# Performance work log

Measured on AMD Instinct MI355X. Metric: run time of the kernel, lower is better.

Reference implementation:

```python
import jax, jax.numpy as jnp
import numpy as np

D_MODEL = 1024
NHEAD = 16
HEAD_DIM = D_MODEL // NHEAD
D_FF = 4096
EPS = 1e-5


def _layer_norm(x, gamma, beta):
    mu = jnp.mean(x, axis=-1, keepdims=True)
    var = jnp.mean((x - mu) ** 2, axis=-1, keepdims=True)
    return (x - mu) * jax.lax.rsqrt(var + EPS) * gamma + beta


def setup_inputs() -> dict:
    key = jax.random.key(0)
    ks = jax.random.split(key, 12)
    B, S = 2, 2048
    s = lambda fan_in: 1.0 / np.sqrt(fan_in)
    return {
        "src": jax.random.normal(ks[0], (B, S, D_MODEL), dtype=jnp.float32),
        "attn_bias": jax.random.normal(ks[1], (NHEAD, S, S), dtype=jnp.float32) * 0.02,
        "qkv_w": jax.random.uniform(ks[2], (3 * D_MODEL, D_MODEL), minval=-s(D_MODEL), maxval=s(D_MODEL)),
        "qkv_b": jax.random.uniform(ks[3], (3 * D_MODEL,), minval=-s(D_MODEL), maxval=s(D_MODEL)),
        "out_w": jax.random.uniform(ks[4], (D_MODEL, D_MODEL), minval=-s(D_MODEL), maxval=s(D_MODEL)),
        "out_b": jax.random.uniform(ks[5], (D_MODEL,), minval=-s(D_MODEL), maxval=s(D_MODEL)),
        "lin1_w": jax.random.uniform(ks[6], (D_FF, D_MODEL), minval=-s(D_MODEL), maxval=s(D_MODEL)),
        "lin1_b": jax.random.uniform(ks[7], (D_FF,), minval=-s(D_MODEL), maxval=s(D_MODEL)),
        "lin2_w": jax.random.uniform(ks[8], (D_MODEL, D_FF), minval=-s(D_FF), maxval=s(D_FF)),
        "lin2_b": jax.random.uniform(ks[9], (D_MODEL,), minval=-s(D_FF), maxval=s(D_FF)),
        "ln1_g": jnp.ones((D_MODEL,)), "ln1_b": jnp.zeros((D_MODEL,)),
        "ln2_g": jnp.ones((D_MODEL,)), "ln2_b": jnp.zeros((D_MODEL,)),
    }


def reference(src, attn_bias, qkv_w, qkv_b, out_w, out_b, lin1_w, lin1_b,
              lin2_w, lin2_b, ln1_g, ln1_b, ln2_g, ln2_b):
    B, S, _ = src.shape
    qkv = src @ qkv_w.T + qkv_b                      # [B,S,3D]
    q, k, v = jnp.split(qkv, 3, axis=-1)
    q = q.reshape(B, S, NHEAD, HEAD_DIM)
    k = k.reshape(B, S, NHEAD, HEAD_DIM)
    v = v.reshape(B, S, NHEAD, HEAD_DIM)
    scores = jnp.einsum('bthd,bshd->bhts', q, k) / np.sqrt(HEAD_DIM)
    scores = scores + attn_bias[None]                # 3D bias -> broadcast over batch
    weights = jax.nn.softmax(scores, axis=-1)
    ctx = jnp.einsum('bhts,bshd->bthd', weights, v).reshape(B, S, D_MODEL)
    attn_out = ctx @ out_w.T + out_b
    x = _layer_norm(src + attn_out, ln1_g, ln1_b)
    ff = jax.nn.gelu(x @ lin1_w.T + lin1_b, approximate=False) @ lin2_w.T + lin2_b
    return _layer_norm(x + ff, ln2_g, ln2_b)
```

## Files before the change

kernel.cpp:

```cpp
#include <hip/hip_runtime.h>
#include <hip/hip_bf16.h>


#define DMODEL 1024
#define NHEAD  16
#define HD     64
#define DFF    4096
#define SEQ    2048
#define BATCH  2
#define TOKD   ((size_t)4096 * 1024)

using short8 = __attribute__((ext_vector_type(8))) short;
using f32x4  = __attribute__((ext_vector_type(4))) float;
typedef unsigned short bfu;

__device__ __forceinline__ bfu f2bf(float f) {
    unsigned int u = __float_as_uint(f);
    unsigned int r = (u + 0x7fffu + ((u >> 16) & 1u)) >> 16;
    return (bfu)r;
}

__device__ __forceinline__ float gelu_exact(float x) {
    return 0.5f * x * (1.0f + erff(x * 0.70710678118654752f));
}

__device__ __forceinline__ void gload16(const void* g, void* l) {
    __builtin_amdgcn_global_load_lds(
        (const __attribute__((address_space(1))) void*)g,
        (__attribute__((address_space(3))) void*)l, 16, 0, 0);
}

__device__ __forceinline__ int swz(int row, int colbyte) {
    return (row * 128 + colbyte) ^ ((row & 7) << 4);
}

__global__ __launch_bounds__(256) void cvt_f32_bf16(const float* __restrict__ in,
                                                    bfu* __restrict__ out, int n4) {
    int i = blockIdx.x * 256 + threadIdx.x;
    if (i >= n4) return;
    float4 v = *(const float4*)(in + (size_t)i * 4);
    uint2 o;
    o.x = (unsigned)f2bf(v.x) | ((unsigned)f2bf(v.y) << 16);
    o.y = (unsigned)f2bf(v.z) | ((unsigned)f2bf(v.w) << 16);
    *(uint2*)(out + (size_t)i * 4) = o;
}

template <int MODE, int BM, int SPLITK>
__global__ __launch_bounds__(256) void gemm_bt(const bfu* __restrict__ A,
                                               const bfu* __restrict__ W,
                                               const float* __restrict__ bias,
                                               void* __restrict__ Cout,
                                               int M, int N, int K) {
    constexpr int MR = BM / 32;
    __shared__ __align__(16) bfu As[BM * 32];
    __shared__ __align__(16) bfu Bs[128 * 32];
    const int tid = threadIdx.x;
    const int wid = tid >> 6, lane = tid & 63;
    const int lg = lane >> 4, li = lane & 15;

    const int nx = gridDim.x;
    int wg = blockIdx.x + nx * blockIdx.y;
    const int nwg = nx * gridDim.y;
    {
        const int qq = nwg >> 3, rr = nwg & 7;
        const int xcd = wg & 7, idx = wg >> 3;
        wg = (xcd < rr ? xcd * (qq + 1) : rr * (qq + 1) + (xcd - rr) * qq) + idx;
    }
    const int row0 = (wg % nx) * BM, col0 = (wg / nx) * 128;
    const int wr = (wid >> 1) * (BM / 2), wc = (wid & 1) * 64;
    f32x4 acc[MR][4] = {};

    const int kchunk = K / SPLITK;
    const int kbeg = blockIdx.z * kchunk;

    const int ch_row = tid >> 2;
    const int ch_col = (tid & 3) * 8;
    const bfu* Ag0 = A + (size_t)(row0 + ch_row) * K + kbeg + ch_col;
    const bfu* Ag1 = A + (size_t)(row0 + 64 + ch_row) * K + kbeg + ch_col;
    const bfu* Wg0 = W + (size_t)(col0 + ch_row) * K + kbeg + ch_col;
    const bfu* Wg1 = W + (size_t)(col0 + 64 + ch_row) * K + kbeg + ch_col;
    char* Al0 = (char*)As + wid * 1024;
    char* Al1 = (char*)As + 4096 + wid * 1024;
    char* Bl0 = (char*)Bs + wid * 1024;
    char* Bl1 = (char*)Bs + 4096 + wid * 1024;

    for (int k0 = 0; k0 < kchunk; k0 += 32) {
        gload16(Ag0 + k0, Al0);
        if constexpr (BM == 128) gload16(Ag1 + k0, Al1);
        gload16(Wg0 + k0, Bl0);
        gload16(Wg1 + k0, Bl1);
        __syncthreads();
        short8 af[MR], bf_[4];
        #pragma unroll
        for (int m = 0; m < MR; ++m)
            af[m] = *(const short8*)(As + (wr + m * 16 + li) * 32 + lg * 8);
        #pragma unroll
        for (int n = 0; n < 4; ++n)
            bf_[n] = *(const short8*)(Bs + (wc + n * 16 + li) * 32 + lg * 8);
        #pragma unroll
        for (int m = 0; m < MR; ++m)
            #pragma unroll
            for (int n = 0; n < 4; ++n)
                acc[m][n] = __builtin_amdgcn_mfma_f32_16x16x32_bf16(af[m], bf_[n], acc[m][n], 0, 0, 0);
        __syncthreads();
    }

    float* Cp3 = (float*)Cout + (size_t)blockIdx.z * M * N;
    #pragma unroll
    for (int m = 0; m < MR; ++m) {
        #pragma unroll
        for (int n = 0; n < 4; ++n) {
            #pragma unroll
            for (int r = 0; r < 4; ++r) {
                int row = row0 + wr + m * 16 + lg * 4 + r;
                int col = col0 + wc + n * 16 + li;
                if (MODE == 3) {
                    Cp3[(size_t)row * N + col] = acc[m][n][r];
                } else {
                    float v = acc[m][n][r] + bias[col];
                    if (MODE == 2) v = gelu_exact(v);
                    ((bfu*)Cout)[(size_t)row * N + col] = f2bf(v);
                }
            }
        }
    }
}

__global__ __launch_bounds__(256) void attn_kernel(const bfu* __restrict__ qkv,
                                                   const float* __restrict__ bias,
                                                   bfu* __restrict__ ctx) {
    __shared__ __align__(16) bfu Ks[128 * 64];
    __shared__ __align__(16) bfu Vt[2][64 * 64];
    __shared__ __align__(16) bfu Ps[4][16 * 64];
    const int tid = threadIdx.x;
    const int wid = tid >> 6, lane = tid & 63;
    const int lg = lane >> 4, li = lane & 15;
    const int q0 = blockIdx.x * 64;
    const int bh = blockIdx.y;
    const int h = bh >> 1, b = bh & 1;
    const size_t tokbase = (size_t)b * SEQ;

    short8 qa[2];
    {
        const bfu* qp = qkv + (tokbase + q0 + wid * 16 + li) * 3072 + h * 64;
        qa[0] = *(const short8*)(qp + lg * 8);
        qa[1] = *(const short8*)(qp + 32 + lg * 8);
    }

    f32x4 o[4] = {};
    float mrow[4], lrow[4];
    #pragma unroll
    for (int r = 0; r < 4; ++r) { mrow[r] = -1e30f; lrow[r] = 0.f; }

    char* pb = (char*)Ps[wid];
    const float* brow = bias + (size_t)h * SEQ * SEQ;
    const int qrbase = q0 + wid * 16 + lg * 4;

    const int krow  = tid >> 3;
    const int kcolb = (tid & 7) * 16;

    for (int kt = 0; kt < SEQ; kt += 128) {
        #pragma unroll
        for (int p = 0; p < 4; ++p) {
            int r_ = p * 32 + krow;
            uint4 v = *(const uint4*)(qkv + (tokbase + kt + r_) * 3072 + 1024 + h * 64 + (kcolb >> 1));
            *(uint4*)((char*)Ks + swz(r_, kcolb)) = v;
        }
        #pragma unroll
        for (int jh = 0; jh < 2; ++jh) {
            #pragma unroll
            for (int i = 0; i < 2; ++i) {
                int jb = i * 4 + wid;
                bfu tmp[8];
                #pragma unroll
                for (int u = 0; u < 8; ++u)
                    tmp[u] = qkv[(tokbase + kt + jh * 64 + jb * 8 + u) * 3072 + 2048 + h * 64 + lane];
                uint4 pv;
                pv.x = (unsigned)tmp[0] | ((unsigned)tmp[1] << 16);
                pv.y = (unsigned)tmp[2] | ((unsigned)tmp[3] << 16);
                pv.z = (unsigned)tmp[4] | ((unsigned)tmp[5] << 16);
                pv.w = (unsigned)tmp[6] | ((unsigned)tmp[7] << 16);
                *(uint4*)((char*)Vt[jh] + swz(lane, jb * 16)) = pv;
            }
        }
        __syncthreads();

        float breg[4][8];
        #pragma unroll
        for (int r = 0; r < 4; ++r) {
            const float* bq = brow + (size_t)(qrbase + r) * SEQ + kt;
            #pragma unroll
            for (int nb = 0; nb < 8; ++nb)
                breg[r][nb] = bq[nb * 16 + li];
        }

        f32x4 s[8] = {};
        __builtin_amdgcn_s_setprio(1);
        #pragma unroll
        for (int cb = 0; cb < 2; ++cb) {
            #pragma unroll
            for (int nb = 0; nb < 8; ++nb) {
                short8 kf = *(const short8*)((char*)Ks + swz(nb * 16 + li, cb * 64 + lg * 16));
                s[nb] = __builtin_amdgcn_mfma_f32_16x16x32_bf16(qa[cb], kf, s[nb], 0, 0, 0);
            }
        }
        __builtin_amdgcn_s_setprio(0);

        #pragma unroll
        for (int r = 0; r < 4; ++r) {
            float sv[8];
            float mx = -1e30f;
            #pragma unroll
            for (int nb = 0; nb < 8; ++nb) {
                float v = s[nb][r] * 0.125f + breg[r][nb];
                sv[nb] = v;
                mx = fmaxf(mx, v);
            }
            #pragma unroll
            for (int off = 8; off; off >>= 1) mx = fmaxf(mx, __shfl_xor(mx, off));
            float mnew = fmaxf(mrow[r], mx);
            float sf = __expf(mrow[r] - mnew);
            mrow[r] = mnew;
            float rs = 0.f;
            #pragma unroll
            for (int nb = 0; nb < 8; ++nb) {
                float p = __expf(sv[nb] - mnew);
                rs += p;
                s[nb][r] = p;
            }
            #pragma unroll
            for (int off = 8; off; off >>= 1) rs += __shfl_xor(rs, off);
            lrow[r] = lrow[r] * sf + rs;
            #pragma unroll
            for (int dc = 0; dc < 4; ++dc) o[dc][r] *= sf;
        }

        #pragma unroll
        for (int jh = 0; jh < 2; ++jh) {
            #pragma unroll
            for (int nb = 0; nb < 4; ++nb)
                #pragma unroll
                for (int r = 0; r < 4; ++r)
                    *(bfu*)(pb + swz(lg * 4 + r, (nb * 16 + li) * 2)) = f2bf(s[jh * 4 + nb][r]);
            __builtin_amdgcn_s_setprio(1);
            #pragma unroll
            for (int jb = 0; jb < 2; ++jb) {
                short8 pa = *(const short8*)(pb + swz(li, jb * 64 + lg * 16));
                short8 vb[4];
                #pragma unroll
                for (int dc = 0; dc < 4; ++dc)
                    vb[dc] = *(const short8*)((char*)Vt[jh] + swz(dc * 16 + li, jb * 64 + lg * 16));
                #pragma unroll
                for (int dc = 0; dc < 4; ++dc)
                    o[dc] = __builtin_amdgcn_mfma_f32_16x16x32_bf16(pa, vb[dc], o[dc], 0, 0, 0);
            }
            __builtin_amdgcn_s_setprio(0);
        }
        __syncthreads();
    }

    #pragma unroll
    for (int dc = 0; dc < 4; ++dc)
        #pragma unroll
        for (int r = 0; r < 4; ++r) {
            int qr = qrbase + r;
            int d = dc * 16 + li;
            float v = o[dc][r] / lrow[r];
            ctx[(tokbase + qr) * 1024 + h * 64 + d] = f2bf(v);
        }
}

template <int P>
__global__ __launch_bounds__(256) void residual_lnP(const float* __restrict__ a,
                                                    const float* __restrict__ parts,
                                                    const float* __restrict__ pbias,
                                                    const float* __restrict__ g,
                                                    const float* __restrict__ be,
                                                    float* __restrict__ xf,
                                                    bfu* __restrict__ xb) {
    const int row = blockIdx.x, t = threadIdx.x;
    const size_t off = (size_t)row * DMODEL + t * 4;
    float4 v = *(const float4*)(a + off);
    #pragma unroll
    for (int i = 0; i < P; ++i) {
        float4 p = *(const float4*)(parts + i * TOKD + off);
        v.x += p.x; v.y += p.y; v.z += p.z; v.w += p.w;
    }
    float4 pb = *(const float4*)(pbias + t * 4);
    v.x += pb.x; v.y += pb.y; v.z += pb.z; v.w += pb.w;

    float s  = v.x + v.y + v.z + v.w;
    float sq = v.x * v.x + v.y * v.y + v.z * v.z + v.w * v.w;
    #pragma unroll
    for (int o2 = 32; o2; o2 >>= 1) { s += __shfl_xor(s, o2); sq += __shfl_xor(sq, o2); }
    __shared__ float red[8];
    const int wid = t >> 6, lane = t & 63;
    if (lane == 0) { red[wid] = s; red[4 + wid] = sq; }
    __syncthreads();
    s  = red[0] + red[1] + red[2] + red[3];
    sq = red[4] + red[5] + red[6] + red[7];
    float mu  = s * (1.0f / DMODEL);
    float var = sq * (1.0f / DMODEL) - mu * mu;
    float rstd = rsqrtf(var + 1e-5f);
    float4 gv  = *(const float4*)(g + t * 4);
    float4 bev = *(const float4*)(be + t * 4);
    float4 ov;
    ov.x = (v.x - mu) * rstd * gv.x + bev.x;
    ov.y = (v.y - mu) * rstd * gv.y + bev.y;
    ov.z = (v.z - mu) * rstd * gv.z + bev.z;
    ov.w = (v.w - mu) * rstd * gv.w + bev.w;
    *(float4*)(xf + off) = ov;
    if (xb) {
        uint2 o;
        o.x = (unsigned)f2bf(ov.x) | ((unsigned)f2bf(ov.y) << 16);
        o.y = (unsigned)f2bf(ov.z) | ((unsigned)f2bf(ov.w) << 16);
        *(uint2*)(xb + off) = o;
    }
}

extern "C" void kernel_launch(void* const* d_in, const int* in_sizes, int n_in,
                              void* d_out, int out_size, void* d_ws, size_t ws_size,
                              hipStream_t stream) {
    const float* src    = (const float*)d_in[0];
    const float* abias  = (const float*)d_in[1];
    const float* qkv_w  = (const float*)d_in[2];
    const float* qkv_b  = (const float*)d_in[3];
    const float* out_w  = (const float*)d_in[4];
    const float* out_b  = (const float*)d_in[5];
    const float* lin1_w = (const float*)d_in[6];
    const float* lin1_b = (const float*)d_in[7];
    const float* lin2_w = (const float*)d_in[8];
    const float* lin2_b = (const float*)d_in[9];
    const float* ln1_g  = (const float*)d_in[10];
    const float* ln1_b  = (const float*)d_in[11];
    const float* ln2_g  = (const float*)d_in[12];
    const float* ln2_b  = (const float*)d_in[13];
    float* out = (float*)d_out;

    const int T = BATCH * SEQ;
    char* w = (char*)d_ws;
    auto take = [&](size_t bytes) { char* p = w; w += (bytes + 255) & ~(size_t)255; return p; };
    bfu*   src_bf  = (bfu*)take((size_t)T * DMODEL * 2);
    bfu*   qkvw_bf = (bfu*)take((size_t)3 * DMODEL * DMODEL * 2);
    bfu*   outw_bf = (bfu*)take((size_t)DMODEL * DMODEL * 2);
    bfu*   l1w_bf  = (bfu*)take((size_t)DFF * DMODEL * 2);
    bfu*   l2w_bf  = (bfu*)take((size_t)DMODEL * DFF * 2);
    bfu*   qkv_bf  = (bfu*)take((size_t)T * 3 * DMODEL * 2);
    bfu*   ctx_bf  = (bfu*)take((size_t)T * DMODEL * 2);
    float* outp_p  = (float*)take((size_t)2 * T * DMODEL * 4);
    float* x_f     = (float*)take((size_t)T * DMODEL * 4);
    bfu*   x_bf    = (bfu*)take((size_t)T * DMODEL * 2);
    bfu*   h1_bf   = (bfu*)take((size_t)T * DFF * 2);
    float* l2_p    = (float*)take((size_t)2 * T * DMODEL * 4);

    auto cvt = [&](const float* in, bfu* o_, size_t n) {
        int n4 = (int)(n / 4);
        cvt_f32_bf16<<<(n4 + 255) / 256, 256, 0, stream>>>(in, o_, n4);
    };
    cvt(src,    src_bf,  (size_t)T * DMODEL);
    cvt(qkv_w,  qkvw_bf, (size_t)3 * DMODEL * DMODEL);
    cvt(out_w,  outw_bf, (size_t)DMODEL * DMODEL);
    cvt(lin1_w, l1w_bf,  (size_t)DFF * DMODEL);
    cvt(lin2_w, l2w_bf,  (size_t)DMODEL * DFF);

    gemm_bt<0, 128, 1><<<dim3(T / 128, (3 * DMODEL) / 128, 1), 256, 0, stream>>>(
        src_bf, qkvw_bf, qkv_b, qkv_bf, T, 3 * DMODEL, DMODEL);
    attn_kernel<<<dim3(SEQ / 64, BATCH * NHEAD), 256, 0, stream>>>(qkv_bf, abias, ctx_bf);
    gemm_bt<3, 64, 2><<<dim3(T / 64, DMODEL / 128, 2), 256, 0, stream>>>(
        ctx_bf, outw_bf, nullptr, outp_p, T, DMODEL, DMODEL);
    residual_lnP<2><<<T, 256, 0, stream>>>(src, outp_p, out_b, ln1_g, ln1_b, x_f, x_bf);
    gemm_bt<2, 128, 1><<<dim3(T / 128, DFF / 128, 1), 256, 0, stream>>>(
        x_bf, l1w_bf, lin1_b, h1_bf, T, DFF, DMODEL);
    gemm_bt<3, 64, 2><<<dim3(T / 64, DMODEL / 128, 2), 256, 0, stream>>>(
        h1_bf, l2w_bf, nullptr, l2_p, T, DMODEL, DFF);
    residual_lnP<2><<<T, 256, 0, stream>>>(x_f, l2_p, lin2_b, ln2_g, ln2_b, out, nullptr);
}
```

Baseline: 383.1 us.

## Double-buffer GEMM LDS tiles and merge weight conversions into one launch

The GEMM now keeps two LDS buffers per operand. It issues the global-to-LDS loads for the next K-slice before running the MFMAs on the current slice, so memory latency overlaps with compute instead of stalling at a barrier each iteration. The five separate fp32-to-bf16 conversion launches become a single kernel that looks up which tensor each thread belongs to from a table of prefix offsets, which removes launch overhead. The trade is doubled LDS use per block, which may lower occupancy, plus a small per-thread index search in the conversion kernel.

```diff
diff --git a/kernel.cpp b/kernel.cpp
--- a/kernel.cpp
+++ b/kernel.cpp
@@ -34,15 +34,24 @@
     return (row * 128 + colbyte) ^ ((row & 7) << 4);
 }
 
-__global__ __launch_bounds__(256) void cvt_f32_bf16(const float* __restrict__ in,
-                                                    bfu* __restrict__ out, int n4) {
-    int i = blockIdx.x * 256 + threadIdx.x;
-    if (i >= n4) return;
-    float4 v = *(const float4*)(in + (size_t)i * 4);
+struct CvtPack {
+    const float* in[5];
+    bfu* out[5];
+    unsigned start[6];
+};
+
+__global__ __launch_bounds__(256) void cvt_multi(CvtPack p) {
+    unsigned gid = blockIdx.x * 256 + threadIdx.x;
+    if (gid >= p.start[5]) return;
+    int i = 0;
+    #pragma unroll
+    for (int k = 1; k < 5; ++k) i += (gid >= p.start[k]);
+    unsigned local = gid - p.start[i];
+    float4 v = *(const float4*)(p.in[i] + (size_t)local * 4);
     uint2 o;
     o.x = (unsigned)f2bf(v.x) | ((unsigned)f2bf(v.y) << 16);
     o.y = (unsigned)f2bf(v.z) | ((unsigned)f2bf(v.w) << 16);
-    *(uint2*)(out + (size_t)i * 4) = o;
+    *(uint2*)(p.out[i] + (size_t)local * 4) = o;
 }
 
 template <int MODE, int BM, int SPLITK>
@@ -52,8 +61,8 @@
                                                void* __restrict__ Cout,
                                                int M, int N, int K) {
     constexpr int MR = BM / 32;
-    __shared__ __align__(16) bfu As[BM * 32];
-    __shared__ __align__(16) bfu Bs[128 * 32];
+    __shared__ __align__(16) bfu As[2][BM * 32];
+    __shared__ __align__(16) bfu Bs[2][128 * 32];
     const int tid = threadIdx.x;
     const int wid = tid >> 6, lane = tid & 63;
     const int lg = lane >> 4, li = lane & 15;
@@ -79,30 +88,33 @@
     const bfu* Ag1 = A + (size_t)(row0 + 64 + ch_row) * K + kbeg + ch_col;
     const bfu* Wg0 = W + (size_t)(col0 + ch_row) * K + kbeg + ch_col;
     const bfu* Wg1 = W + (size_t)(col0 + 64 + ch_row) * K + kbeg + ch_col;
-    char* Al0 = (char*)As + wid * 1024;
-    char* Al1 = (char*)As + 4096 + wid * 1024;
-    char* Bl0 = (char*)Bs + wid * 1024;
-    char* Bl1 = (char*)Bs + 4096 + wid * 1024;
-
+
+    auto stage = [&](int buf, int k0) {
+        gload16(Ag0 + k0, (char*)As[buf] + wid * 1024);
+        if constexpr (BM == 128) gload16(Ag1 + k0, (char*)As[buf] + 4096 + wid * 1024);
+        gload16(Wg0 + k0, (char*)Bs[buf] + wid * 1024);
+        gload16(Wg1 + k0, (char*)Bs[buf] + 4096 + wid * 1024);
+    };
+
+    stage(0, 0);
+    __syncthreads();
+    int cur = 0;
     for (int k0 = 0; k0 < kchunk; k0 += 32) {
-        gload16(Ag0 + k0, Al0);
-        if constexpr (BM == 128) gload16(Ag1 + k0, Al1);
-        gload16(Wg0 + k0, Bl0);
-        gload16(Wg1 + k0, Bl1);
-        __syncthreads();
+        if (k0 + 32 < kchunk) stage(cur ^ 1, k0 + 32);
         short8 af[MR], bf_[4];
         #pragma unroll
         for (int m = 0; m < MR; ++m)
-            af[m] = *(const short8*)(As + (wr + m * 16 + li) * 32 + lg * 8);
+            af[m] = *(const short8*)(As[cur] + (wr + m * 16 + li) * 32 + lg * 8);
         #pragma unroll
         for (int n = 0; n < 4; ++n)
-            bf_[n] = *(const short8*)(Bs + (wc + n * 16 + li) * 32 + lg * 8);
+            bf_[n] = *(const short8*)(Bs[cur] + (wc + n * 16 + li) * 32 + lg * 8);
         #pragma unroll
         for (int m = 0; m < MR; ++m)
             #pragma unroll
             for (int n = 0; n < 4; ++n)
                 acc[m][n] = __builtin_amdgcn_mfma_f32_16x16x32_bf16(af[m], bf_[n], acc[m][n], 0, 0, 0);
         __syncthreads();
+        cur ^= 1;
     }
 
     float* Cp3 = (float*)Cout + (size_t)blockIdx.z * M * N;
@@ -353,15 +365,23 @@
     bfu*   h1_bf   = (bfu*)take((size_t)T * DFF * 2);
     float* l2_p    = (float*)take((size_t)2 * T * DMODEL * 4);
 
-    auto cvt = [&](const float* in, bfu* o_, size_t n) {
-        int n4 = (int)(n / 4);
-        cvt_f32_bf16<<<(n4 + 255) / 256, 256, 0, stream>>>(in, o_, n4);
-    };
-    cvt(src,    src_bf,  (size_t)T * DMODEL);
-    cvt(qkv_w,  qkvw_bf, (size_t)3 * DMODEL * DMODEL);
-    cvt(out_w,  outw_bf, (size_t)DMODEL * DMODEL);
-    cvt(lin1_w, l1w_bf,  (size_t)DFF * DMODEL);
-    cvt(lin2_w, l2w_bf,  (size_t)DMODEL * DFF);
+    {
+        CvtPack p;
+        p.in[0] = src;    p.out[0] = src_bf;
+        p.in[1] = qkv_w;  p.out[1] = qkvw_bf;
+        p.in[2] = out_w;  p.out[2] = outw_bf;
+        p.in[3] = lin1_w; p.out[3] = l1w_bf;
+        p.in[4] = lin2_w; p.out[4] = l2w_bf;
+        unsigned n4[5] = {
+            (unsigned)((size_t)T * DMODEL / 4),
+            (unsigned)((size_t)3 * DMODEL * DMODEL / 4),
+            (unsigned)((size_t)DMODEL * DMODEL / 4),
+            (unsigned)((size_t)DFF * DMODEL / 4),
+            (unsigned)((size_t)DMODEL * DFF / 4)};
+        p.start[0] = 0;
+        for (int i = 0; i < 5; ++i) p.start[i + 1] = p.start[i] + n4[i];
+        cvt_multi<<<(p.start[5] + 255) / 256, 256, 0, stream>>>(p);
+    }
 
     gemm_bt<0, 128, 1><<<dim3(T / 128, (3 * DMODEL) / 128, 1), 256, 0, stream>>>(
         src_bf, qkvw_bf, qkv_b, qkv_bf, T, 3 * DMODEL, DMODEL);
```

After: 364.5 us. 4.9% less time.
